# Optimization experiments

Measured on AMD Instinct MI355X. Metric: run time of the kernel, lower is better.

## Reference

```python
import jax, jax.numpy as jnp
import numpy as np

N_NODES = 50000
N_EDGES = 600000
H = 128
EPSILON = 0.7071067811865476  # layer residual scaling
EPS = 1e-08                   # norm stabilizer


def _mlp(x, W1, b1, W2, b2):
    # Linear -> silu -> Linear (blocks=2 context network)
    h = jax.nn.silu(x @ W1 + b1)
    return h @ W2 + b2


def setup_inputs() -> dict:
    key = jax.random.key(0)
    ks = jax.random.split(key, 12)
    def xav(k, fan_in, shape):
        return jax.random.normal(k, shape, jnp.float32) / jnp.sqrt(jnp.float32(fan_in))
    dir_raw = jax.random.normal(ks[2], (N_EDGES, 3), jnp.float32)
    dir_ij = dir_raw / jnp.linalg.norm(dir_raw, axis=-1, keepdims=True)
    return {
        "s": jax.random.normal(ks[0], (N_NODES, 1, H), jnp.float32),
        "v": jax.random.normal(ks[1], (N_NODES, 3, H), jnp.float32),
        "dir_ij": dir_ij,
        "Wij": jax.random.normal(ks[3], (N_EDGES, 1, 3 * H), jnp.float32),
        "senders": jax.random.randint(ks[4], (N_EDGES,), 0, N_NODES),
        "receivers": jax.random.randint(ks[5], (N_EDGES,), 0, N_NODES),
        "Wi1": xav(ks[6], H, (H, H)),
        "bi1": jnp.zeros((H,), jnp.float32),
        "Wi2": xav(ks[7], H, (H, 3 * H)),
        "bi2": jnp.zeros((3 * H,), jnp.float32),
        "Wm1": xav(ks[8], 2 * H, (2 * H, H)),
        "bm1": jnp.zeros((H,), jnp.float32),
        "Wm2": xav(ks[9], H, (H, 3 * H)),
        "bm2": jnp.zeros((3 * H,), jnp.float32),
        "Wvm": xav(ks[10], H, (H, 2 * H)),
    }


def reference(s, v, dir_ij, Wij, senders, receivers,
              Wi1, bi1, Wi2, bi2, Wm1, bm1, Wm2, bm2, Wvm):
    n_nodes = s.shape[0]
    # ---- message (inter-particle) ----
    x = _mlp(s, Wi1, bi1, Wi2, bi2)           # (N, 1, 3H)
    xj = x[receivers]                          # (E, 1, 3H) gather
    vj = v[receivers]                          # (E, 3, H)  gather
    ds_e, dv1, dv2 = jnp.split(Wij * xj, 3, axis=-1)   # each (E, 1, H)
    dv_e = dv1 * dir_ij[..., jnp.newaxis] + dv2 * vj   # (E, 3, H)
    ds = jax.ops.segment_sum(ds_e, senders, num_segments=n_nodes)
    dv = jax.ops.segment_sum(dv_e, senders, num_segments=n_nodes)
    s = (s + ds) * EPSILON
    v = (v + dv) * EPSILON
    # ---- update (intra-particle) ----
    v_l, v_r = jnp.split(v @ Wvm, 2, axis=-1)          # (N, 3, H) each
    v_norm = jnp.sqrt(jnp.sum(v_r ** 2, axis=-2, keepdims=True) + EPS)  # (N,1,H)
    ts = jnp.concatenate([s, v_norm], axis=-1)         # (N, 1, 2H)
    ds_u, dv_u, dsv = jnp.split(_mlp(ts, Wm1, bm1, Wm2, bm2), 3, axis=-1)
    dv_u = v_l * dv_u
    dsv = dsv * jnp.sum(v_r * v_l, axis=1, keepdims=True)
    s = (s + ds_u + dsv) * EPSILON                     # (N, 1, H)
    v = (v + dv_u) * EPSILON                           # (N, 3, H)
    # pack (s, v) into a single array along axis 1 -> (N, 4, H)
    return jnp.concatenate([s, v], axis=1)
```

## Files before the change

### kernel.cpp

```cpp
#include <hip/hip_runtime.h>

#define H 128
#define EPSILON 0.7071067811865476f
#define NEPS 1e-8f

typedef short bf16x8 __attribute__((ext_vector_type(8)));
typedef float f32x4 __attribute__((ext_vector_type(4)));
typedef unsigned short ushort_t;

__device__ __forceinline__ float silu_f(float x) {
    return x / (1.0f + __expf(-x));
}
__device__ __forceinline__ unsigned short bfround(float w) {
    unsigned ub = __float_as_uint(w);
    return (unsigned short)((ub + 0x7FFF + ((ub >> 16) & 1)) >> 16);
}
__device__ __forceinline__ float bfu(unsigned short u) { return __uint_as_float(((unsigned)u) << 16); }

__device__ __forceinline__ void pack_one(const float* __restrict__ W, int N,
                                         ushort_t* __restrict__ p, int tid) {
    int CT = N >> 4;
    int j = tid & 7;
    int l = (tid >> 3) & 63;
    int rest = tid >> 9;
    int ct = rest % CT;
    int ks = rest / CT;
    int row = ks * 32 + ((l >> 4) << 3) + j;
    int col = ct * 16 + (l & 15);
    p[tid] = bfround(W[(size_t)row * N + col]);
}

__global__ void k_prep(const float* __restrict__ Wi1, const float* __restrict__ Wi2,
                       const float* __restrict__ Wvm, const float* __restrict__ Wm1,
                       const float* __restrict__ Wm2,
                       ushort_t* __restrict__ Wi1p, ushort_t* __restrict__ Wi2p,
                       ushort_t* __restrict__ Wvp, ushort_t* __restrict__ Wm1p,
                       ushort_t* __restrict__ Wm2p,
                       const float4* __restrict__ v4, ushort_t* __restrict__ xv,
                       int* __restrict__ cnt, int n_cnt, int n4) {
    int gid = blockIdx.x * blockDim.x + threadIdx.x;
    int stride = gridDim.x * blockDim.x;
    int S0 = n_cnt;
    int S1 = S0 + 16384;
    int S2 = S1 + 49152;
    int S3 = S2 + 32768;
    int S4 = S3 + 32768;
    int S5 = S4 + 49152;
    int S6 = S5 + n4;
    for (int i = gid; i < S6; i += stride) {
        if (i < S0)      cnt[i] = 0;
        else if (i < S1) pack_one(Wi1, 128, Wi1p, i - S0);
        else if (i < S2) pack_one(Wi2, 384, Wi2p, i - S1);
        else if (i < S3) pack_one(Wvm, 256, Wvp,  i - S2);
        else if (i < S4) pack_one(Wm1, 128, Wm1p, i - S3);
        else if (i < S5) pack_one(Wm2, 384, Wm2p, i - S4);
        else {
            int j = i - S5;
            int node = j / 96, part = j - node * 96;
            float4 f = v4[j];
            ushort4 u;
            u.x = bfround(f.x); u.y = bfround(f.y); u.z = bfround(f.z); u.w = bfround(f.w);
            *(ushort4*)&xv[(size_t)node * 768 + 384 + 4 * part] = u;
        }
    }
}

__global__ __launch_bounds__(256, 6) void k1_mfma(
        const float* __restrict__ s,
        const ushort_t* __restrict__ W1p, const ushort_t* __restrict__ W2p,
        const float* __restrict__ bi1, const float* __restrict__ bi2,
        ushort_t* __restrict__ xv, int n_nodes) {
    __shared__ ushort_t Ab[16 * 136];
    __shared__ ushort_t Hb[16 * 136];
    int t = threadIdx.x;
    int node0 = blockIdx.x * 16;
    int wv = t >> 6, lane = t & 63;
    int g = lane >> 4, cl = lane & 15;

    #pragma unroll
    for (int i = 0; i < 8; ++i) {
        int flat = t + i * 256;
        int n = flat >> 7, k = flat & 127;
        int node = node0 + n; if (node >= n_nodes) node = n_nodes - 1;
        Ab[n * 136 + k] = bfround(s[(size_t)node * 128 + k]);
    }
    __syncthreads();

    f32x4 acc1[2] = {};
    #pragma unroll
    for (int ks = 0; ks < 4; ++ks) {
        bf16x8 ah = *(const bf16x8*)&Ab[cl * 136 + ks * 32 + g * 8];
        #pragma unroll
        for (int c = 0; c < 2; ++c) {
            int ct = wv * 2 + c;
            bf16x8 bh = *(const bf16x8*)&W1p[((size_t)(ks * 8 + ct) * 64 + lane) * 8];
            acc1[c] = __builtin_amdgcn_mfma_f32_16x16x32_bf16(ah, bh, acc1[c], 0, 0, 0);
        }
    }
    #pragma unroll
    for (int c = 0; c < 2; ++c) {
        int col = (wv * 2 + c) * 16 + cl;
        float bias = bi1[col];
        #pragma unroll
        for (int r = 0; r < 4; ++r) {
            int row = g * 4 + r;
            Hb[row * 136 + col] = bfround(silu_f(acc1[c][r] + bias));
        }
    }
    __syncthreads();

    f32x4 acc2[6] = {};
    #pragma unroll
    for (int ks = 0; ks < 4; ++ks) {
        bf16x8 ah = *(const bf16x8*)&Hb[cl * 136 + ks * 32 + g * 8];
        #pragma unroll
        for (int c = 0; c < 6; ++c) {
            int ct = wv * 6 + c;
            bf16x8 bh = *(const bf16x8*)&W2p[((size_t)(ks * 24 + ct) * 64 + lane) * 8];
            acc2[c] = __builtin_amdgcn_mfma_f32_16x16x32_bf16(ah, bh, acc2[c], 0, 0, 0);
        }
    }
    #pragma unroll
    for (int c = 0; c < 6; ++c) {
        int col = (wv * 6 + c) * 16 + cl;
        float bias = bi2[col];
        #pragma unroll
        for (int r = 0; r < 4; ++r) {
            int node = node0 + g * 4 + r;
            if (node < n_nodes) xv[(size_t)node * 768 + col] = bfround(acc2[c][r] + bias);
        }
    }
}

__global__ void k_hist(const int* __restrict__ senders, int* __restrict__ cnt, int n_edges) {
    int e = blockIdx.x * blockDim.x + threadIdx.x;
    if (e < n_edges) atomicAdd(&cnt[senders[e]], 1);
}

__global__ void k_alloc(const int* __restrict__ cnt, int* __restrict__ starts,
                        int* __restrict__ head, int* __restrict__ cursor, int n) {
    int i = blockIdx.x * blockDim.x + threadIdx.x;
    int lane = threadIdx.x & 63;
    int c = (i < n) ? cnt[i] : 0;
    int pref = c;
    #pragma unroll
    for (int off = 1; off < 64; off <<= 1) {
        int up = __shfl_up(pref, off, 64);
        if (lane >= off) pref += up;
    }
    int total = __shfl(pref, 63, 64);
    int base = 0;
    if (lane == 63) base = atomicAdd(cursor, total);
    base = __shfl(base, 63, 64);
    if (i < n) { int p = base + pref - c; starts[i] = p; head[i] = p; }
}

__global__ void k_scatter(const int* __restrict__ senders, const int* __restrict__ receivers,
                          int* __restrict__ head, int2* __restrict__ epair, int n_edges) {
    int e = blockIdx.x * blockDim.x + threadIdx.x;
    if (e < n_edges) {
        int p = atomicAdd(&head[senders[e]], 1);
        int2 pr; pr.x = e; pr.y = receivers[e];
        epair[p] = pr;
    }
}

__global__ __launch_bounds__(256) void k2_csr(
        const float4* __restrict__ s4, const ushort_t* __restrict__ xv,
        const float* __restrict__ dir, const float4* __restrict__ w4,
        const int* __restrict__ starts, const int* __restrict__ cnt,
        const int2* __restrict__ epair, ushort_t* __restrict__ mid, int n_nodes) {
    __shared__ float4 red[8][128];
    int node = blockIdx.x;
    int t = threadIdx.x;
    int slot = t >> 5, lane = t & 31;
    int beg = starts[node], num = cnt[node];
    float4 ds  = {0.f, 0.f, 0.f, 0.f};
    float4 dv0 = {0.f, 0.f, 0.f, 0.f};
    float4 dv1 = {0.f, 0.f, 0.f, 0.f};
    float4 dv2 = {0.f, 0.f, 0.f, 0.f};
    for (int q = slot; q < num; q += 8) {
        int2 er = epair[beg + q];
        int e = er.x, r = er.y;
        const float4*   we  = w4 + (size_t)e * 96;
        const ushort_t* xvr = xv + (size_t)r * 768;
        float4 wa = we[lane], wb = we[32 + lane], wc = we[64 + lane];
        ushort4 xa = *(const ushort4*)&xvr[4 * lane];
        ushort4 xb = *(const ushort4*)&xvr[128 + 4 * lane];
        ushort4 xc = *(const ushort4*)&xvr[256 + 4 * lane];
        ushort4 va = *(const ushort4*)&xvr[384 + 4 * lane];
        ushort4 vb = *(const ushort4*)&xvr[512 + 4 * lane];
        ushort4 vc = *(const ushort4*)&xvr[640 + 4 * lane];
        float d0 = dir[3 * (size_t)e + 0];
        float d1 = dir[3 * (size_t)e + 1];
        float d2 = dir[3 * (size_t)e + 2];
        float bx = wb.x * bfu(xb.x), by = wb.y * bfu(xb.y), bz = wb.z * bfu(xb.z), bw = wb.w * bfu(xb.w);
        float cx = wc.x * bfu(xc.x), cy = wc.y * bfu(xc.y), cz = wc.z * bfu(xc.z), cw = wc.w * bfu(xc.w);
        ds.x += wa.x * bfu(xa.x); ds.y += wa.y * bfu(xa.y);
        ds.z += wa.z * bfu(xa.z); ds.w += wa.w * bfu(xa.w);
        dv0.x += bx * d0 + cx * bfu(va.x); dv0.y += by * d0 + cy * bfu(va.y);
        dv0.z += bz * d0 + cz * bfu(va.z); dv0.w += bw * d0 + cw * bfu(va.w);
        dv1.x += bx * d1 + cx * bfu(vb.x); dv1.y += by * d1 + cy * bfu(vb.y);
        dv1.z += bz * d1 + cz * bfu(vb.z); dv1.w += bw * d1 + cw * bfu(vb.w);
        dv2.x += bx * d2 + cx * bfu(vc.x); dv2.y += by * d2 + cy * bfu(vc.y);
        dv2.z += bz * d2 + cz * bfu(vc.z); dv2.w += bw * d2 + cw * bfu(vc.w);
    }
    red[slot][lane]      = ds;
    red[slot][32 + lane] = dv0;
    red[slot][64 + lane] = dv1;
    red[slot][96 + lane] = dv2;
    __syncthreads();
    if (t < 128) {
        float4 acc = red[0][t];
        #pragma unroll
        for (int q2 = 1; q2 < 8; ++q2) {
            float4 r2 = red[q2][t];
            acc.x += r2.x; acc.y += r2.y; acc.z += r2.z; acc.w += r2.w;
        }
        int which = t >> 5, hh = t & 31;
        float4 base;
        if (which == 0) {
            base = s4[(size_t)node * 32 + hh];
        } else {
            ushort4 u = *(const ushort4*)&xv[(size_t)node * 768 + 384 + (size_t)(which - 1) * 128 + 4 * hh];
            base.x = bfu(u.x); base.y = bfu(u.y); base.z = bfu(u.z); base.w = bfu(u.w);
        }
        ushort4 o;
        o.x = bfround((base.x + acc.x) * EPSILON);
        o.y = bfround((base.y + acc.y) * EPSILON);
        o.z = bfround((base.z + acc.z) * EPSILON);
        o.w = bfround((base.w + acc.w) * EPSILON);
        *(ushort4*)&mid[(size_t)node * 512 + 4 * t] = o;
    }
}

__global__ __launch_bounds__(256, 3) void k3_mfma(
        const ushort_t* __restrict__ mid,
        const ushort_t* __restrict__ Wvp, const ushort_t* __restrict__ W1p,
        const ushort_t* __restrict__ W2p,
        const float* __restrict__ bm1, const float* __restrict__ bm2,
        float* __restrict__ out, int n_nodes) {
    __shared__ __align__(16) char pool[51968];
    ushort_t* Ab  = (ushort_t*)pool;
    ushort_t* vlb = (ushort_t*)(pool + 13056);
    ushort_t* vrc = (ushort_t*)(pool + 26112);
    ushort_t* Tb  = (ushort_t*)(pool + 39168);
    ushort_t* Hb  = (ushort_t*)(pool + 47616);
    float* C3 = (float*)(pool + 26112);

    int t = threadIdx.x;
    int node0 = blockIdx.x * 16;
    int wv = t >> 6, lane = t & 63;
    int g = lane >> 4, cl = lane & 15;

    float smid_reg[8], dot_reg[8];

    #pragma unroll
    for (int i = 0; i < 6; ++i) {
        int flat4 = t + i * 256;
        int row = flat4 >> 5, k4 = flat4 & 31;
        int n = row / 3, d = row - n * 3;
        int node = node0 + n; if (node >= n_nodes) node = n_nodes - 1;
        ushort4 u = *(const ushort4*)&mid[(size_t)node * 512 + (size_t)(1 + d) * 128 + 4 * k4];
        *(ushort4*)&Ab[row * 136 + 4 * k4] = u;
    }
    #pragma unroll
    for (int i = 0; i < 8; ++i) {
        int flat = t + i * 256;
        int n = flat >> 7, k = flat & 127;
        int node = node0 + n; if (node >= n_nodes) node = n_nodes - 1;
        smid_reg[i] = bfu(mid[(size_t)node * 512 + k]);
    }
    __syncthreads();

    #pragma unroll
    for (int rt = 0; rt < 3; ++rt) {
        bf16x8 ah[4];
        #pragma unroll
        for (int ks = 0; ks < 4; ++ks)
            ah[ks] = *(const bf16x8*)&Ab[(rt * 16 + cl) * 136 + ks * 32 + g * 8];
        f32x4 acc[4] = {};
        #pragma unroll
        for (int ks = 0; ks < 4; ++ks) {
            #pragma unroll
            for (int c = 0; c < 4; ++c) {
                int ct = wv * 4 + c;
                bf16x8 bh = *(const bf16x8*)&Wvp[((size_t)(ks * 16 + ct) * 64 + lane) * 8];
                acc[c] = __builtin_amdgcn_mfma_f32_16x16x32_bf16(ah[ks], bh, acc[c], 0, 0, 0);
            }
        }
        #pragma unroll
        for (int c = 0; c < 4; ++c) {
            int col = (wv * 4 + c) * 16 + cl;
            ushort_t* dst = (col < 128) ? vlb : vrc;
            int cc = col & 127;
            #pragma unroll
            for (int r = 0; r < 4; ++r)
                dst[(rt * 16 + g * 4 + r) * 136 + cc] = bfround(acc[c][r]);
        }
    }
    __syncthreads();

    #pragma unroll
    for (int i = 0; i < 8; ++i) {
        int flat = t + i * 256;
        int n = flat >> 7, h = flat & 127;
        float r0 = bfu(vrc[(3 * n + 0) * 136 + h]);
        float r1 = bfu(vrc[(3 * n + 1) * 136 + h]);
        float r2 = bfu(vrc[(3 * n + 2) * 136 + h]);
        float l0 = bfu(vlb[(3 * n + 0) * 136 + h]);
        float l1 = bfu(vlb[(3 * n + 1) * 136 + h]);
        float l2 = bfu(vlb[(3 * n + 2) * 136 + h]);
        float nrm = sqrtf(r0 * r0 + r1 * r1 + r2 * r2 + NEPS);
        dot_reg[i] = r0 * l0 + r1 * l1 + r2 * l2;
        Tb[n * 264 + 128 + h] = bfround(nrm);
        Tb[n * 264 + h] = bfround(smid_reg[i]);
    }
    __syncthreads();

    f32x4 acc2[2] = {};
    #pragma unroll
    for (int ks = 0; ks < 8; ++ks) {
        bf16x8 ah = *(const bf16x8*)&Tb[cl * 264 + ks * 32 + g * 8];
        #pragma unroll
        for (int c = 0; c < 2; ++c) {
            int ct = wv * 2 + c;
            bf16x8 bh = *(const bf16x8*)&W1p[((size_t)(ks * 8 + ct) * 64 + lane) * 8];
            acc2[c] = __builtin_amdgcn_mfma_f32_16x16x32_bf16(ah, bh, acc2[c], 0, 0, 0);
        }
    }
    #pragma unroll
    for (int c = 0; c < 2; ++c) {
        int col = (wv * 2 + c) * 16 + cl;
        float bias = bm1[col];
        #pragma unroll
        for (int r = 0; r < 4; ++r) {
            int row = g * 4 + r;
            Hb[row * 136 + col] = bfround(silu_f(acc2[c][r] + bias));
        }
    }
    __syncthreads();

    f32x4 acc3[6] = {};
    #pragma unroll
    for (int ks = 0; ks < 4; ++ks) {
        bf16x8 ah = *(const bf16x8*)&Hb[cl * 136 + ks * 32 + g * 8];
        #pragma unroll
        for (int c = 0; c < 6; ++c) {
            int ct = wv * 6 + c;
            bf16x8 bh = *(const bf16x8*)&W2p[((size_t)(ks * 24 + ct) * 64 + lane) * 8];
            acc3[c] = __builtin_amdgcn_mfma_f32_16x16x32_bf16(ah, bh, acc3[c], 0, 0, 0);
        }
    }
    __syncthreads();
    #pragma unroll
    for (int c = 0; c < 6; ++c) {
        int col = (wv * 6 + c) * 16 + cl;
        float bias = bm2[col];
        #pragma unroll
        for (int r = 0; r < 4; ++r)
            C3[(g * 4 + r) * 400 + col] = acc3[c][r] + bias;
    }
    __syncthreads();

    #pragma unroll
    for (int i = 0; i < 8; ++i) {
        int flat = t + i * 256;
        int n = flat >> 7, h = flat & 127;
        int node = node0 + n;
        if (node >= n_nodes) continue;
        float ds_u = C3[n * 400 + h];
        float dv_u = C3[n * 400 + 128 + h];
        float dsv  = C3[n * 400 + 256 + h] * dot_reg[i];
        out[(size_t)node * 512 + h] = (smid_reg[i] + ds_u + dsv) * EPSILON;
        #pragma unroll
        for (int d = 0; d < 3; ++d) {
            int row = 3 * n + d;
            float vmid = bfu(Ab[row * 136 + h]);
            float vl_v = bfu(vlb[row * 136 + h]);
            out[(size_t)node * 512 + 128 + d * 128 + h] = (vmid + vl_v * dv_u) * EPSILON;
        }
    }
}

static inline size_t align_up(size_t x, size_t a) { return (x + a - 1) / a * a; }

extern "C" void kernel_launch(void* const* d_in, const int* in_sizes, int n_in,
                              void* d_out, int out_size, void* d_ws, size_t ws_size,
                              hipStream_t stream) {
    const float* s       = (const float*)d_in[0];
    const float* v       = (const float*)d_in[1];
    const float* dir     = (const float*)d_in[2];
    const float* Wij     = (const float*)d_in[3];
    const int*   senders = (const int*)d_in[4];
    const int*   recv    = (const int*)d_in[5];
    const float* Wi1     = (const float*)d_in[6];
    const float* bi1     = (const float*)d_in[7];
    const float* Wi2     = (const float*)d_in[8];
    const float* bi2     = (const float*)d_in[9];
    const float* Wm1     = (const float*)d_in[10];
    const float* bm1     = (const float*)d_in[11];
    const float* Wm2     = (const float*)d_in[12];
    const float* bm2     = (const float*)d_in[13];
    const float* Wvm     = (const float*)d_in[14];

    int n_nodes = in_sizes[0] / H;
    int n_edges = in_sizes[4];
    float* out = (float*)d_out;

    char* ws = (char*)d_ws;
    size_t off = 0;
    ushort_t* xv  = (ushort_t*)(ws + off); off = align_up(off + (size_t)n_nodes * 768 * 2, 256);
    ushort_t* mid = (ushort_t*)(ws + off); off = align_up(off + (size_t)n_nodes * 512 * 2, 256);
    int* starts = (int*)(ws + off); off = align_up(off + (size_t)n_nodes * 4, 256);
    int* cnt    = (int*)(ws + off); off = align_up(off + (size_t)(n_nodes + 1) * 4, 256);
    int* cursor = cnt + n_nodes;
    int* head   = (int*)(ws + off); off = align_up(off + (size_t)n_nodes * 4, 256);
    int2* epair = (int2*)(ws + off); off = align_up(off + (size_t)n_edges * 8, 256);
    ushort_t* Wi1p = (ushort_t*)(ws + off); off = align_up(off + 16384 * 2, 256);
    ushort_t* Wi2p = (ushort_t*)(ws + off); off = align_up(off + 49152 * 2, 256);
    ushort_t* Wvp  = (ushort_t*)(ws + off); off = align_up(off + 32768 * 2, 256);
    ushort_t* Wm1p = (ushort_t*)(ws + off); off = align_up(off + 32768 * 2, 256);
    ushort_t* Wm2p = (ushort_t*)(ws + off); off = align_up(off + 49152 * 2, 256);
    if (off > ws_size) return;

    int n4 = n_nodes * 96;
    int prep_total = (n_nodes + 1) + 16384 + 49152 + 32768 + 32768 + 49152 + n4;
    int prep_blocks = (prep_total + 255) / 256;
    if (prep_blocks > 2048) prep_blocks = 2048;
    k_prep<<<prep_blocks, 256, 0, stream>>>(
        Wi1, Wi2, Wvm, Wm1, Wm2, Wi1p, Wi2p, Wvp, Wm1p, Wm2p,
        (const float4*)v, xv, cnt, n_nodes + 1, n4);

    k_hist<<<(n_edges + 255) / 256, 256, 0, stream>>>(senders, cnt, n_edges);
    k_alloc<<<(n_nodes + 255) / 256, 256, 0, stream>>>(cnt, starts, head, cursor, n_nodes);
    k_scatter<<<(n_edges + 255) / 256, 256, 0, stream>>>(senders, recv, head, epair, n_edges);

    k1_mfma<<<(n_nodes + 15) / 16, 256, 0, stream>>>(
        s, Wi1p, Wi2p, bi1, bi2, xv, n_nodes);

    k2_csr<<<n_nodes, 256, 0, stream>>>(
        (const float4*)s, xv, dir,
        (const float4*)Wij, starts, cnt, epair, mid, n_nodes);

    k3_mfma<<<(n_nodes + 15) / 16, 256, 0, stream>>>(
        mid, Wvp, Wm1p, Wm2p, bm1, bm2, out, n_nodes);
}
```

Measured before the change: 476.8 us.

## Fuse v bf16 conversion into k1, pre-sort edge dirs, add nontemporal loads/stores

```diff
diff --git a/kernel.cpp b/kernel.cpp
--- a/kernel.cpp
+++ b/kernel.cpp
@@ -36,8 +36,7 @@
                        ushort_t* __restrict__ Wi1p, ushort_t* __restrict__ Wi2p,
                        ushort_t* __restrict__ Wvp, ushort_t* __restrict__ Wm1p,
                        ushort_t* __restrict__ Wm2p,
-                       const float4* __restrict__ v4, ushort_t* __restrict__ xv,
-                       int* __restrict__ cnt, int n_cnt, int n4) {
+                       int* __restrict__ cnt, int n_cnt) {
     int gid = blockIdx.x * blockDim.x + threadIdx.x;
     int stride = gridDim.x * blockDim.x;
     int S0 = n_cnt;
@@ -46,27 +45,18 @@
     int S3 = S2 + 32768;
     int S4 = S3 + 32768;
     int S5 = S4 + 49152;
-    int S6 = S5 + n4;
-    for (int i = gid; i < S6; i += stride) {
+    for (int i = gid; i < S5; i += stride) {
         if (i < S0)      cnt[i] = 0;
         else if (i < S1) pack_one(Wi1, 128, Wi1p, i - S0);
         else if (i < S2) pack_one(Wi2, 384, Wi2p, i - S1);
         else if (i < S3) pack_one(Wvm, 256, Wvp,  i - S2);
         else if (i < S4) pack_one(Wm1, 128, Wm1p, i - S3);
-        else if (i < S5) pack_one(Wm2, 384, Wm2p, i - S4);
-        else {
-            int j = i - S5;
-            int node = j / 96, part = j - node * 96;
-            float4 f = v4[j];
-            ushort4 u;
-            u.x = bfround(f.x); u.y = bfround(f.y); u.z = bfround(f.z); u.w = bfround(f.w);
-            *(ushort4*)&xv[(size_t)node * 768 + 384 + 4 * part] = u;
-        }
+        else             pack_one(Wm2, 384, Wm2p, i - S4);
     }
 }
 
 __global__ __launch_bounds__(256, 6) void k1_mfma(
-        const float* __restrict__ s,
+        const float* __restrict__ s, const float4* __restrict__ v4,
         const ushort_t* __restrict__ W1p, const ushort_t* __restrict__ W2p,
         const float* __restrict__ bi1, const float* __restrict__ bi2,
         ushort_t* __restrict__ xv, int n_nodes) {
@@ -130,6 +120,19 @@
             if (node < n_nodes) xv[(size_t)node * 768 + col] = bfround(acc2[c][r] + bias);
         }
     }
+
+    #pragma unroll
+    for (int i = 0; i < 6; ++i) {
+        int flat = t + i * 256;
+        int n = flat / 96, part = flat - n * 96;
+        int node = node0 + n;
+        if (node < n_nodes) {
+            float4 f = v4[(size_t)node * 96 + part];
+            ushort4 u;
+            u.x = bfround(f.x); u.y = bfround(f.y); u.z = bfround(f.z); u.w = bfround(f.w);
+            *(ushort4*)&xv[(size_t)node * 768 + 384 + 4 * part] = u;
+        }
+    }
 }
 
 __global__ void k_hist(const int* __restrict__ senders, int* __restrict__ cnt, int n_edges) {
@@ -156,20 +159,26 @@
 }
 
 __global__ void k_scatter(const int* __restrict__ senders, const int* __restrict__ receivers,
-                          int* __restrict__ head, int2* __restrict__ epair, int n_edges) {
+                          const float* __restrict__ dir, int* __restrict__ head,
+                          int* __restrict__ eord, float4* __restrict__ edir, int n_edges) {
     int e = blockIdx.x * blockDim.x + threadIdx.x;
     if (e < n_edges) {
         int p = atomicAdd(&head[senders[e]], 1);
-        int2 pr; pr.x = e; pr.y = receivers[e];
-        epair[p] = pr;
+        eord[p] = e;
+        float4 ed;
+        ed.x = dir[3 * (size_t)e + 0];
+        ed.y = dir[3 * (size_t)e + 1];
+        ed.z = dir[3 * (size_t)e + 2];
+        ed.w = __int_as_float(receivers[e]);
+        edir[p] = ed;
     }
 }
 
 __global__ __launch_bounds__(256) void k2_csr(
         const float4* __restrict__ s4, const ushort_t* __restrict__ xv,
-        const float* __restrict__ dir, const float4* __restrict__ w4,
-        const int* __restrict__ starts, const int* __restrict__ cnt,
-        const int2* __restrict__ epair, ushort_t* __restrict__ mid, int n_nodes) {
+        const float* __restrict__ wf, const int* __restrict__ starts,
+        const int* __restrict__ cnt, const int* __restrict__ eord,
+        const float4* __restrict__ edir, ushort_t* __restrict__ mid, int n_nodes) {
     __shared__ float4 red[8][128];
     int node = blockIdx.x;
     int t = threadIdx.x;
@@ -180,30 +189,30 @@
     float4 dv1 = {0.f, 0.f, 0.f, 0.f};
     float4 dv2 = {0.f, 0.f, 0.f, 0.f};
     for (int q = slot; q < num; q += 8) {
-        int2 er = epair[beg + q];
-        int e = er.x, r = er.y;
-        const float4*   we  = w4 + (size_t)e * 96;
+        int e = eord[beg + q];
+        float4 ed = edir[beg + q];
+        int r = __float_as_int(ed.w);
+        const f32x4*    we  = (const f32x4*)(wf + (size_t)e * 384);
         const ushort_t* xvr = xv + (size_t)r * 768;
-        float4 wa = we[lane], wb = we[32 + lane], wc = we[64 + lane];
+        f32x4 wa = __builtin_nontemporal_load(we + lane);
+        f32x4 wb = __builtin_nontemporal_load(we + 32 + lane);
+        f32x4 wc = __builtin_nontemporal_load(we + 64 + lane);
         ushort4 xa = *(const ushort4*)&xvr[4 * lane];
         ushort4 xb = *(const ushort4*)&xvr[128 + 4 * lane];
         ushort4 xc = *(const ushort4*)&xvr[256 + 4 * lane];
         ushort4 va = *(const ushort4*)&xvr[384 + 4 * lane];
         ushort4 vb = *(const ushort4*)&xvr[512 + 4 * lane];
         ushort4 vc = *(const ushort4*)&xvr[640 + 4 * lane];
-        float d0 = dir[3 * (size_t)e + 0];
-        float d1 = dir[3 * (size_t)e + 1];
-        float d2 = dir[3 * (size_t)e + 2];
-        float bx = wb.x * bfu(xb.x), by = wb.y * bfu(xb.y), bz = wb.z * bfu(xb.z), bw = wb.w * bfu(xb.w);
-        float cx = wc.x * bfu(xc.x), cy = wc.y * bfu(xc.y), cz = wc.z * bfu(xc.z), cw = wc.w * bfu(xc.w);
-        ds.x += wa.x * bfu(xa.x); ds.y += wa.y * bfu(xa.y);
-        ds.z += wa.z * bfu(xa.z); ds.w += wa.w * bfu(xa.w);
-        dv0.x += bx * d0 + cx * bfu(va.x); dv0.y += by * d0 + cy * bfu(va.y);
-        dv0.z += bz * d0 + cz * bfu(va.z); dv0.w += bw * d0 + cw * bfu(va.w);
-        dv1.x += bx * d1 + cx * bfu(vb.x); dv1.y += by * d1 + cy * bfu(vb.y);
-        dv1.z += bz * d1 + cz * bfu(vb.z); dv1.w += bw * d1 + cw * bfu(vb.w);
-        dv2.x += bx * d2 + cx * bfu(vc.x); dv2.y += by * d2 + cy * bfu(vc.y);
-        dv2.z += bz * d2 + cz * bfu(vc.z); dv2.w += bw * d2 + cw * bfu(vc.w);
+        float bx = wb[0] * bfu(xb.x), by = wb[1] * bfu(xb.y), bz = wb[2] * bfu(xb.z), bw = wb[3] * bfu(xb.w);
+        float cx = wc[0] * bfu(xc.x), cy = wc[1] * bfu(xc.y), cz = wc[2] * bfu(xc.z), cw = wc[3] * bfu(xc.w);
+        ds.x += wa[0] * bfu(xa.x); ds.y += wa[1] * bfu(xa.y);
+        ds.z += wa[2] * bfu(xa.z); ds.w += wa[3] * bfu(xa.w);
+        dv0.x += bx * ed.x + cx * bfu(va.x); dv0.y += by * ed.x + cy * bfu(va.y);
+        dv0.z += bz * ed.x + cz * bfu(va.z); dv0.w += bw * ed.x + cw * bfu(va.w);
+        dv1.x += bx * ed.y + cx * bfu(vb.x); dv1.y += by * ed.y + cy * bfu(vb.y);
+        dv1.z += bz * ed.y + cz * bfu(vb.z); dv1.w += bw * ed.y + cw * bfu(vb.w);
+        dv2.x += bx * ed.z + cx * bfu(vc.x); dv2.y += by * ed.z + cy * bfu(vc.y);
+        dv2.z += bz * ed.z + cz * bfu(vc.z); dv2.w += bw * ed.z + cw * bfu(vc.w);
     }
     red[slot][lane]      = ds;
     red[slot][32 + lane] = dv0;
@@ -372,13 +381,15 @@
         float ds_u = C3[n * 400 + h];
         float dv_u = C3[n * 400 + 128 + h];
         float dsv  = C3[n * 400 + 256 + h] * dot_reg[i];
-        out[(size_t)node * 512 + h] = (smid_reg[i] + ds_u + dsv) * EPSILON;
+        __builtin_nontemporal_store((smid_reg[i] + ds_u + dsv) * EPSILON,
+                                    &out[(size_t)node * 512 + h]);
         #pragma unroll
         for (int d = 0; d < 3; ++d) {
             int row = 3 * n + d;
             float vmid = bfu(Ab[row * 136 + h]);
             float vl_v = bfu(vlb[row * 136 + h]);
-            out[(size_t)node * 512 + 128 + d * 128 + h] = (vmid + vl_v * dv_u) * EPSILON;
+            __builtin_nontemporal_store((vmid + vl_v * dv_u) * EPSILON,
+                                        &out[(size_t)node * 512 + 128 + d * 128 + h]);
         }
     }
 }
@@ -416,7 +427,8 @@
     int* cnt    = (int*)(ws + off); off = align_up(off + (size_t)(n_nodes + 1) * 4, 256);
     int* cursor = cnt + n_nodes;
     int* head   = (int*)(ws + off); off = align_up(off + (size_t)n_nodes * 4, 256);
-    int2* epair = (int2*)(ws + off); off = align_up(off + (size_t)n_edges * 8, 256);
+    int* eord   = (int*)(ws + off); off = align_up(off + (size_t)n_edges * 4, 256);
+    float4* edir = (float4*)(ws + off); off = align_up(off + (size_t)n_edges * 16, 256);
     ushort_t* Wi1p = (ushort_t*)(ws + off); off = align_up(off + 16384 * 2, 256);
     ushort_t* Wi2p = (ushort_t*)(ws + off); off = align_up(off + 49152 * 2, 256);
     ushort_t* Wvp  = (ushort_t*)(ws + off); off = align_up(off + 32768 * 2, 256);
@@ -424,24 +436,19 @@
     ushort_t* Wm2p = (ushort_t*)(ws + off); off = align_up(off + 49152 * 2, 256);
     if (off > ws_size) return;
 
-    int n4 = n_nodes * 96;
-    int prep_total = (n_nodes + 1) + 16384 + 49152 + 32768 + 32768 + 49152 + n4;
-    int prep_blocks = (prep_total + 255) / 256;
-    if (prep_blocks > 2048) prep_blocks = 2048;
-    k_prep<<<prep_blocks, 256, 0, stream>>>(
-        Wi1, Wi2, Wvm, Wm1, Wm2, Wi1p, Wi2p, Wvp, Wm1p, Wm2p,
-        (const float4*)v, xv, cnt, n_nodes + 1, n4);
+    int prep_total = (n_nodes + 1) + 16384 + 49152 + 32768 + 32768 + 49152;
+    k_prep<<<(prep_total + 255) / 256, 256, 0, stream>>>(
+        Wi1, Wi2, Wvm, Wm1, Wm2, Wi1p, Wi2p, Wvp, Wm1p, Wm2p, cnt, n_nodes + 1);
 
     k_hist<<<(n_edges + 255) / 256, 256, 0, stream>>>(senders, cnt, n_edges);
     k_alloc<<<(n_nodes + 255) / 256, 256, 0, stream>>>(cnt, starts, head, cursor, n_nodes);
-    k_scatter<<<(n_edges + 255) / 256, 256, 0, stream>>>(senders, recv, head, epair, n_edges);
+    k_scatter<<<(n_edges + 255) / 256, 256, 0, stream>>>(senders, recv, dir, head, eord, edir, n_edges);
 
     k1_mfma<<<(n_nodes + 15) / 16, 256, 0, stream>>>(
-        s, Wi1p, Wi2p, bi1, bi2, xv, n_nodes);
+        s, (const float4*)v, Wi1p, Wi2p, bi1, bi2, xv, n_nodes);
 
     k2_csr<<<n_nodes, 256, 0, stream>>>(
-        (const float4*)s, xv, dir,
-        (const float4*)Wij, starts, cnt, epair, mid, n_nodes);
+        (const float4*)s, xv, Wij, starts, cnt, eord, edir, mid, n_nodes);
 
     k3_mfma<<<(n_nodes + 15) / 16, 256, 0, stream>>>(
         mid, Wvp, Wm1p, Wm2p, bm1, bm2, out, n_nodes);
```

After: 452.0 us. 1.05x faster.
